# Kernel optimization log

Hardware: AMD Instinct MI355X
Metric: run time of the kernel (lower is better)

## Reference

```python
import jax, jax.numpy as jnp
import numpy as np

NU, NV = 8192, 8192
IN_DIM, HID, NCLS = 128, 64, 5


def setup_inputs() -> dict:
    key = jax.random.key(0)
    k1, k2, k3, k4, k5, k6, k7 = jax.random.split(key, 7)
    return {
        "u": jax.random.normal(k1, (NU, IN_DIM), dtype=jnp.float32),
        "v": jax.random.normal(k2, (NV, IN_DIM), dtype=jnp.float32),
        "adj": jax.random.uniform(k3, (NU, NV), dtype=jnp.float32),
        "degree": jax.random.uniform(k4, (NU + NV,), dtype=jnp.float32),
        "u_weight": jax.random.normal(k5, (NCLS, IN_DIM, HID), dtype=jnp.float32),
        "v_weight": jax.random.normal(k6, (NCLS, IN_DIM, HID), dtype=jnp.float32),
        "bias": jax.random.normal(k7, (HID,), dtype=jnp.float32),
        "r": 4,
    }


def reference(u, v, adj, degree, u_weight, v_weight, bias, r):
    # Sum weight slices for rating classes 0..r (r is a static Python int).
    Wu = jnp.sum(u_weight[: r + 1], axis=0)  # [IN_DIM, HID]
    Wv = jnp.sum(v_weight[: r + 1], axis=0)
    # Dropout is identity at p=0.0 (eval mode).
    su = u @ Wu  # [NU, HID]
    sv = v @ Wv  # [NV, HID]
    nu = adj.shape[0]
    # Block adjacency [[0, A], [A^T, 0]] row-scaled by diag(degree), applied to
    # concat(su, sv) -- computed block-wise, same math without the dense block matrix.
    top = degree[:nu, None] * (adj @ sv)      # [NU, HID]
    bot = degree[nu:, None] * (adj.T @ su)    # [NV, HID]
    return jnp.concatenate([top, bot], axis=0) + bias
```

## Files before the change

### kernel.cpp

```cpp
#include <hip/hip_runtime.h>
#include <stdint.h>


#define HID 64
#define IN_DIM 128
#define NROWS 8192
#define NCLS 5

typedef float f32x4 __attribute__((ext_vector_type(4)));
typedef short s16x8 __attribute__((ext_vector_type(8)));
typedef unsigned short u16;

static __device__ __forceinline__ short f2b(float x) {
    unsigned u = __builtin_bit_cast(unsigned, x);
    return (short)((u + 0x7FFFu + ((u >> 16) & 1u)) >> 16);
}

__global__ __launch_bounds__(256, 2) void k_prep(
    const float* __restrict__ u, const float* __restrict__ v,
    const float* __restrict__ uw, const float* __restrict__ vw,
    const int* __restrict__ rp, u16* __restrict__ ws)
{
    __shared__ float W[IN_DIM * HID];
    __shared__ float X[64 * 129];

    const int y = blockIdx.y;
    const float* __restrict__ src  = y ? v  : u;
    const float* __restrict__ wsrc = y ? vw : uw;
    u16* __restrict__ dstT = ws + (size_t)y * (HID * NROWS);
    const int i0 = blockIdx.x * 64;
    const int t = threadIdx.x;
    int r = *rp; if (r > NCLS - 1) r = NCLS - 1; if (r < 0) r = 0;

    for (int idx = t; idx < IN_DIM * HID; idx += 256) {
        float s = 0.f;
        for (int c = 0; c <= r; ++c) s += wsrc[c * (IN_DIM * HID) + idx];
        W[idx] = s;
    }
    #pragma unroll
    for (int qq = 0; qq < 8; ++qq) {
        int idx = t + qq * 256;
        int row = idx >> 5, c4 = idx & 31;
        f32x4 val = *(const f32x4*)&src[(size_t)(i0 + row) * IN_DIM + c4 * 4];
        float* d = &X[row * 129 + c4 * 4];
        d[0] = val[0]; d[1] = val[1]; d[2] = val[2]; d[3] = val[3];
    }
    __syncthreads();

    const int i = t & 63, h0 = (t >> 6) * 16;
    float acc[16];
    #pragma unroll
    for (int k = 0; k < 16; ++k) acc[k] = 0.f;
    for (int c = 0; c < IN_DIM; ++c) {
        float uv = X[i * 129 + c];
        const f32x4* wr = (const f32x4*)&W[c * HID + h0];
        f32x4 w0 = wr[0], w1 = wr[1], w2 = wr[2], w3 = wr[3];
        acc[0]  += uv * w0[0]; acc[1]  += uv * w0[1];
        acc[2]  += uv * w0[2]; acc[3]  += uv * w0[3];
        acc[4]  += uv * w1[0]; acc[5]  += uv * w1[1];
        acc[6]  += uv * w1[2]; acc[7]  += uv * w1[3];
        acc[8]  += uv * w2[0]; acc[9]  += uv * w2[1];
        acc[10] += uv * w2[2]; acc[11] += uv * w2[3];
        acc[12] += uv * w3[0]; acc[13] += uv * w3[1];
        acc[14] += uv * w3[2]; acc[15] += uv * w3[3];
    }
    #pragma unroll
    for (int hh = 0; hh < 16; ++hh)
        dstT[(size_t)(h0 + hh) * NROWS + i0 + i] = (u16)f2b(acc[hh]);
}

__global__ __launch_bounds__(256, 2) void k_main(
    const float* __restrict__ adj, const float* __restrict__ degree,
    const float* __restrict__ bias, const u16* __restrict__ ws,
    float* __restrict__ out)
{
    __shared__ float S[4][64 * 33];

    const int mode = blockIdx.y;
    const int bx = blockIdx.x;
    const int t = threadIdx.x;
    const int w = t >> 6, l = t & 63;
    const int q = l >> 4, l15 = l & 15;
    const int m0 = bx * 32;
    const unsigned a = (unsigned)(bx >> 1);
    const int kbase = w * 2048;
    const u16* __restrict__ BT = ws + (mode == 0 ? (size_t)(HID * NROWS) : 0);

    f32x4 acc[2][4];
    #pragma unroll
    for (int i = 0; i < 2; ++i)
        #pragma unroll
        for (int j = 0; j < 4; ++j) acc[i][j] = (f32x4){0.f, 0.f, 0.f, 0.f};

    if (mode == 0) {
        const float* __restrict__ ap0 = adj + (size_t)(m0 + l15) * NROWS;
        const float* __restrict__ ap1 = ap0 + (size_t)16 * NROWS;
        for (int tau = 0; tau < 32; ++tau) {
            const int k0 = kbase + (int)(((a + tau) & 31u) << 6);
            #pragma unroll
            for (int kh = 0; kh < 2; ++kh) {
                const int k = k0 + kh * 32 + q * 8;
                f32x4 a00 = *(const f32x4*)(ap0 + k);
                f32x4 a01 = *(const f32x4*)(ap0 + k + 4);
                f32x4 a10 = *(const f32x4*)(ap1 + k);
                f32x4 a11 = *(const f32x4*)(ap1 + k + 4);
                s16x8 bf[4];
                #pragma unroll
                for (int nn = 0; nn < 4; ++nn)
                    bf[nn] = *(const s16x8*)(BT + (size_t)(nn * 16 + l15) * NROWS + k);
                s16x8 af0, af1;
                af0[0]=f2b(a00[0]); af0[1]=f2b(a00[1]); af0[2]=f2b(a00[2]); af0[3]=f2b(a00[3]);
                af0[4]=f2b(a01[0]); af0[5]=f2b(a01[1]); af0[6]=f2b(a01[2]); af0[7]=f2b(a01[3]);
                af1[0]=f2b(a10[0]); af1[1]=f2b(a10[1]); af1[2]=f2b(a10[2]); af1[3]=f2b(a10[3]);
                af1[4]=f2b(a11[0]); af1[5]=f2b(a11[1]); af1[6]=f2b(a11[2]); af1[7]=f2b(a11[3]);
                #pragma unroll
                for (int nn = 0; nn < 4; ++nn) {
                    acc[0][nn] = __builtin_amdgcn_mfma_f32_16x16x32_bf16(af0, bf[nn], acc[0][nn], 0, 0, 0);
                    acc[1][nn] = __builtin_amdgcn_mfma_f32_16x16x32_bf16(af1, bf[nn], acc[1][nn], 0, 0, 0);
                }
            }
        }
    } else {
        float* __restrict__ T = S[w];
        const int wr_r = l >> 3;
        const int wr_c = (l & 7) * 4;
        const float* __restrict__ cb = adj + m0 + wr_c;
        for (int tau = 0; tau < 32; ++tau) {
            const int i0 = kbase + (int)(((a - tau) & 31u) << 6);
            f32x4 tr[8];
            #pragma unroll
            for (int c = 0; c < 8; ++c)
                tr[c] = *(const f32x4*)(cb + (size_t)(i0 + c * 8 + wr_r) * NROWS);
            #pragma unroll
            for (int c = 0; c < 8; ++c) {
                float* d = &T[(c * 8 + wr_r) * 33 + wr_c];
                d[0] = tr[c][0]; d[1] = tr[c][1]; d[2] = tr[c][2]; d[3] = tr[c][3];
            }
            asm volatile("s_waitcnt lgkmcnt(0)" ::: "memory");
            #pragma unroll
            for (int kh = 0; kh < 2; ++kh) {
                const int kk = i0 + kh * 32 + q * 8;
                s16x8 bf[4];
                #pragma unroll
                for (int nn = 0; nn < 4; ++nn)
                    bf[nn] = *(const s16x8*)(BT + (size_t)(nn * 16 + l15) * NROWS + kk);
                s16x8 af[2];
                #pragma unroll
                for (int mt = 0; mt < 2; ++mt) {
                    const int j = mt * 16 + l15;
                    #pragma unroll
                    for (int tt = 0; tt < 8; ++tt)
                        af[mt][tt] = f2b(T[(kh * 32 + q * 8 + tt) * 33 + j]);
                }
                #pragma unroll
                for (int nn = 0; nn < 4; ++nn) {
                    acc[0][nn] = __builtin_amdgcn_mfma_f32_16x16x32_bf16(af[0], bf[nn], acc[0][nn], 0, 0, 0);
                    acc[1][nn] = __builtin_amdgcn_mfma_f32_16x16x32_bf16(af[1], bf[nn], acc[1][nn], 0, 0, 0);
                }
            }
            asm volatile("" ::: "memory");
        }
    }

    asm volatile("" ::: "memory");
    {
        float* __restrict__ P = S[w];
        #pragma unroll
        for (int mt = 0; mt < 2; ++mt)
            #pragma unroll
            for (int nn = 0; nn < 4; ++nn)
                #pragma unroll
                for (int rg = 0; rg < 4; ++rg)
                    P[(mt * 16 + q * 4 + rg) * 64 + nn * 16 + l15] = acc[mt][nn][rg];
    }
    __syncthreads();

    const int e0 = t * 8;
    const int m = e0 >> 6, n = e0 & 63;
    f32x4 s0 = (f32x4){0.f,0.f,0.f,0.f}, s1 = s0;
    #pragma unroll
    for (int ww = 0; ww < 4; ++ww) {
        s0 += *(const f32x4*)&S[ww][e0];
        s1 += *(const f32x4*)&S[ww][e0 + 4];
    }
    const int grow = (mode ? NROWS : 0) + m0 + m;
    const float d = degree[grow];
    f32x4 b0 = *(const f32x4*)&bias[n];
    f32x4 b1 = *(const f32x4*)&bias[n + 4];
    f32x4 o0 = d * s0 + b0;
    f32x4 o1 = d * s1 + b1;
    *(f32x4*)&out[(size_t)grow * HID + n]     = o0;
    *(f32x4*)&out[(size_t)grow * HID + n + 4] = o1;
}

extern "C" void kernel_launch(void* const* d_in, const int* in_sizes, int n_in,
                              void* d_out, int out_size, void* d_ws, size_t ws_size,
                              hipStream_t stream) {
    (void)in_sizes; (void)n_in; (void)out_size; (void)ws_size;
    const float* u      = (const float*)d_in[0];
    const float* v      = (const float*)d_in[1];
    const float* adj    = (const float*)d_in[2];
    const float* degree = (const float*)d_in[3];
    const float* uw     = (const float*)d_in[4];
    const float* vw     = (const float*)d_in[5];
    const float* bias   = (const float*)d_in[6];
    const int*   rp     = (const int*)d_in[7];
    u16*   ws  = (u16*)d_ws;
    float* out = (float*)d_out;

    k_prep<<<dim3(128, 2), 256, 0, stream>>>(u, v, uw, vw, rp, ws);
    k_main<<<dim3(256, 2), 256, 0, stream>>>(adj, degree, bias, ws, out);
}
```

Before: 481.6 us.

## Read adj once, emit bf16 transposed tiles for the bottom product

The fused two-mode kernel is split into k_top and k_bot. k_top streams fp32 adj rows once for adj@sv, converts them to bf16, transposes them through swizzled LDS, and writes a blocked bf16 copy of adj^T to workspace. k_bot then computes adj^T@su from that half-size bf16 copy instead of rereading fp32 adj with column-strided loads. The top path also prefetches the next tile into registers and shrinks row tiles to 16. The cost is an extra 128MB bf16 write plus read, one more launch, and a dependency between the two kernels.

```diff
diff --git a/kernel.cpp b/kernel.cpp
--- a/kernel.cpp
+++ b/kernel.cpp
@@ -69,128 +69,175 @@
         dstT[(size_t)(h0 + hh) * NROWS + i0 + i] = (u16)f2b(acc[hh]);
 }
 
-__global__ __launch_bounds__(256, 2) void k_main(
+__global__ __launch_bounds__(256, 2) void k_top(
     const float* __restrict__ adj, const float* __restrict__ degree,
     const float* __restrict__ bias, const u16* __restrict__ ws,
-    float* __restrict__ out)
+    u16* __restrict__ wt, float* __restrict__ out)
 {
-    __shared__ float S[4][64 * 33];
-
-    const int mode = blockIdx.y;
+    __shared__ u16  Tt[4][16 * 64];
+    __shared__ float S[4][16 * 64];
+
     const int bx = blockIdx.x;
     const int t = threadIdx.x;
     const int w = t >> 6, l = t & 63;
     const int q = l >> 4, l15 = l & 15;
-    const int m0 = bx * 32;
-    const unsigned a = (unsigned)(bx >> 1);
+    const int m0 = bx * 16;
     const int kbase = w * 2048;
-    const u16* __restrict__ BT = ws + (mode == 0 ? (size_t)(HID * NROWS) : 0);
-
-    f32x4 acc[2][4];
-    #pragma unroll
-    for (int i = 0; i < 2; ++i)
-        #pragma unroll
-        for (int j = 0; j < 4; ++j) acc[i][j] = (f32x4){0.f, 0.f, 0.f, 0.f};
-
-    if (mode == 0) {
-        const float* __restrict__ ap0 = adj + (size_t)(m0 + l15) * NROWS;
-        const float* __restrict__ ap1 = ap0 + (size_t)16 * NROWS;
-        for (int tau = 0; tau < 32; ++tau) {
-            const int k0 = kbase + (int)(((a + tau) & 31u) << 6);
-            #pragma unroll
-            for (int kh = 0; kh < 2; ++kh) {
-                const int k = k0 + kh * 32 + q * 8;
-                f32x4 a00 = *(const f32x4*)(ap0 + k);
-                f32x4 a01 = *(const f32x4*)(ap0 + k + 4);
-                f32x4 a10 = *(const f32x4*)(ap1 + k);
-                f32x4 a11 = *(const f32x4*)(ap1 + k + 4);
-                s16x8 bf[4];
-                #pragma unroll
-                for (int nn = 0; nn < 4; ++nn)
-                    bf[nn] = *(const s16x8*)(BT + (size_t)(nn * 16 + l15) * NROWS + k);
-                s16x8 af0, af1;
-                af0[0]=f2b(a00[0]); af0[1]=f2b(a00[1]); af0[2]=f2b(a00[2]); af0[3]=f2b(a00[3]);
-                af0[4]=f2b(a01[0]); af0[5]=f2b(a01[1]); af0[6]=f2b(a01[2]); af0[7]=f2b(a01[3]);
-                af1[0]=f2b(a10[0]); af1[1]=f2b(a10[1]); af1[2]=f2b(a10[2]); af1[3]=f2b(a10[3]);
-                af1[4]=f2b(a11[0]); af1[5]=f2b(a11[1]); af1[6]=f2b(a11[2]); af1[7]=f2b(a11[3]);
-                #pragma unroll
-                for (int nn = 0; nn < 4; ++nn) {
-                    acc[0][nn] = __builtin_amdgcn_mfma_f32_16x16x32_bf16(af0, bf[nn], acc[0][nn], 0, 0, 0);
-                    acc[1][nn] = __builtin_amdgcn_mfma_f32_16x16x32_bf16(af1, bf[nn], acc[1][nn], 0, 0, 0);
-                }
-            }
-        }
-    } else {
-        float* __restrict__ T = S[w];
-        const int wr_r = l >> 3;
-        const int wr_c = (l & 7) * 4;
-        const float* __restrict__ cb = adj + m0 + wr_c;
-        for (int tau = 0; tau < 32; ++tau) {
-            const int i0 = kbase + (int)(((a - tau) & 31u) << 6);
-            f32x4 tr[8];
-            #pragma unroll
-            for (int c = 0; c < 8; ++c)
-                tr[c] = *(const f32x4*)(cb + (size_t)(i0 + c * 8 + wr_r) * NROWS);
-            #pragma unroll
-            for (int c = 0; c < 8; ++c) {
-                float* d = &T[(c * 8 + wr_r) * 33 + wr_c];
-                d[0] = tr[c][0]; d[1] = tr[c][1]; d[2] = tr[c][2]; d[3] = tr[c][3];
-            }
-            asm volatile("s_waitcnt lgkmcnt(0)" ::: "memory");
-            #pragma unroll
-            for (int kh = 0; kh < 2; ++kh) {
-                const int kk = i0 + kh * 32 + q * 8;
-                s16x8 bf[4];
-                #pragma unroll
-                for (int nn = 0; nn < 4; ++nn)
-                    bf[nn] = *(const s16x8*)(BT + (size_t)(nn * 16 + l15) * NROWS + kk);
-                s16x8 af[2];
-                #pragma unroll
-                for (int mt = 0; mt < 2; ++mt) {
-                    const int j = mt * 16 + l15;
-                    #pragma unroll
-                    for (int tt = 0; tt < 8; ++tt)
-                        af[mt][tt] = f2b(T[(kh * 32 + q * 8 + tt) * 33 + j]);
-                }
-                #pragma unroll
-                for (int nn = 0; nn < 4; ++nn) {
-                    acc[0][nn] = __builtin_amdgcn_mfma_f32_16x16x32_bf16(af[0], bf[nn], acc[0][nn], 0, 0, 0);
-                    acc[1][nn] = __builtin_amdgcn_mfma_f32_16x16x32_bf16(af[1], bf[nn], acc[1][nn], 0, 0, 0);
-                }
-            }
-            asm volatile("" ::: "memory");
-        }
+    const u16* __restrict__ BT = ws + (size_t)HID * NROWS;
+    const float* __restrict__ ap0 = adj + (size_t)(m0 + l15) * NROWS + q * 8;
+    u16* __restrict__ Tw = Tt[w];
+
+    f32x4 acc[4];
+    #pragma unroll
+    for (int nn = 0; nn < 4; ++nn) acc[nn] = (f32x4){0.f, 0.f, 0.f, 0.f};
+
+    f32x4 c00 = *(const f32x4*)(ap0 + kbase);
+    f32x4 c01 = *(const f32x4*)(ap0 + kbase + 4);
+    f32x4 c10 = *(const f32x4*)(ap0 + kbase + 32);
+    f32x4 c11 = *(const f32x4*)(ap0 + kbase + 36);
+
+    for (int tau = 0; tau < 32; ++tau) {
+        const int k0c = kbase + tau * 64;
+        const int knx = kbase + ((tau + 1) & 31) * 64;
+        f32x4 n00 = *(const f32x4*)(ap0 + knx);
+        f32x4 n01 = *(const f32x4*)(ap0 + knx + 4);
+        f32x4 n10 = *(const f32x4*)(ap0 + knx + 32);
+        f32x4 n11 = *(const f32x4*)(ap0 + knx + 36);
+
+        s16x8 af0;
+        af0[0]=f2b(c00[0]); af0[1]=f2b(c00[1]); af0[2]=f2b(c00[2]); af0[3]=f2b(c00[3]);
+        af0[4]=f2b(c01[0]); af0[5]=f2b(c01[1]); af0[6]=f2b(c01[2]); af0[7]=f2b(c01[3]);
+        *(s16x8*)&Tw[l15 * 64 + ((q ^ (l15 & 7)) * 8)] = af0;
+        {
+            s16x8 bf[4];
+            #pragma unroll
+            for (int nn = 0; nn < 4; ++nn)
+                bf[nn] = *(const s16x8*)(BT + (size_t)(nn * 16 + l15) * NROWS + k0c + q * 8);
+            #pragma unroll
+            for (int nn = 0; nn < 4; ++nn)
+                acc[nn] = __builtin_amdgcn_mfma_f32_16x16x32_bf16(af0, bf[nn], acc[nn], 0, 0, 0);
+        }
+        s16x8 af1;
+        af1[0]=f2b(c10[0]); af1[1]=f2b(c10[1]); af1[2]=f2b(c10[2]); af1[3]=f2b(c10[3]);
+        af1[4]=f2b(c11[0]); af1[5]=f2b(c11[1]); af1[6]=f2b(c11[2]); af1[7]=f2b(c11[3]);
+        *(s16x8*)&Tw[l15 * 64 + (((4 + q) ^ (l15 & 7)) * 8)] = af1;
+        {
+            s16x8 bf[4];
+            #pragma unroll
+            for (int nn = 0; nn < 4; ++nn)
+                bf[nn] = *(const s16x8*)(BT + (size_t)(nn * 16 + l15) * NROWS + k0c + 32 + q * 8);
+            #pragma unroll
+            for (int nn = 0; nn < 4; ++nn)
+                acc[nn] = __builtin_amdgcn_mfma_f32_16x16x32_bf16(af1, bf[nn], acc[nn], 0, 0, 0);
+        }
+
+        asm volatile("s_waitcnt lgkmcnt(0)" ::: "memory");
+
+        s16x8 p0, p1;
+        #pragma unroll
+        for (int ii = 0; ii < 8; ++ii)
+            p0[ii] = (short)Tw[ii * 64 + (((l >> 3) ^ ii) & 7) * 8 + (l & 7)];
+        #pragma unroll
+        for (int ii = 0; ii < 8; ++ii)
+            p1[ii] = (short)Tw[(ii + 8) * 64 + (((l >> 3) ^ ii) & 7) * 8 + (l & 7)];
+
+        u16* dst = wt + (size_t)((k0c >> 4) + (l >> 4)) * (NROWS * 16)
+                      + (size_t)bx * 256 + (size_t)(l & 15) * 16;
+        *(s16x8*)dst       = p0;
+        *(s16x8*)(dst + 8) = p1;
+
+        asm volatile("" ::: "memory");
+        c00 = n00; c01 = n01; c10 = n10; c11 = n11;
     }
 
     asm volatile("" ::: "memory");
     {
         float* __restrict__ P = S[w];
         #pragma unroll
-        for (int mt = 0; mt < 2; ++mt)
-            #pragma unroll
-            for (int nn = 0; nn < 4; ++nn)
-                #pragma unroll
-                for (int rg = 0; rg < 4; ++rg)
-                    P[(mt * 16 + q * 4 + rg) * 64 + nn * 16 + l15] = acc[mt][nn][rg];
+        for (int nn = 0; nn < 4; ++nn)
+            #pragma unroll
+            for (int rg = 0; rg < 4; ++rg)
+                P[(q * 4 + rg) * 64 + nn * 16 + l15] = acc[nn][rg];
     }
     __syncthreads();
 
-    const int e0 = t * 8;
+    const int e0 = t * 4;
     const int m = e0 >> 6, n = e0 & 63;
-    f32x4 s0 = (f32x4){0.f,0.f,0.f,0.f}, s1 = s0;
-    #pragma unroll
-    for (int ww = 0; ww < 4; ++ww) {
-        s0 += *(const f32x4*)&S[ww][e0];
-        s1 += *(const f32x4*)&S[ww][e0 + 4];
-    }
-    const int grow = (mode ? NROWS : 0) + m0 + m;
+    f32x4 s = (f32x4){0.f, 0.f, 0.f, 0.f};
+    #pragma unroll
+    for (int ww = 0; ww < 4; ++ww) s += *(const f32x4*)&S[ww][e0];
+    const int grow = m0 + m;
     const float d = degree[grow];
-    f32x4 b0 = *(const f32x4*)&bias[n];
-    f32x4 b1 = *(const f32x4*)&bias[n + 4];
-    f32x4 o0 = d * s0 + b0;
-    f32x4 o1 = d * s1 + b1;
-    *(f32x4*)&out[(size_t)grow * HID + n]     = o0;
-    *(f32x4*)&out[(size_t)grow * HID + n + 4] = o1;
+    f32x4 b = *(const f32x4*)&bias[n];
+    *(f32x4*)&out[(size_t)grow * HID + n] = d * s + b;
+}
+
+__global__ __launch_bounds__(256, 2) void k_bot(
+    const float* __restrict__ degree, const float* __restrict__ bias,
+    const u16* __restrict__ ws, const u16* __restrict__ wt,
+    float* __restrict__ out)
+{
+    __shared__ float S[4][16 * 64];
+
+    const int bx = blockIdx.x;
+    const int t = threadIdx.x;
+    const int w = t >> 6, l = t & 63;
+    const int q = l >> 4, l15 = l & 15;
+    const int m0 = bx * 16;
+    const int kbase = w * 2048;
+    const u16* __restrict__ BT = ws;
+    const u16* __restrict__ PB = wt + (size_t)bx * (NROWS * 16)
+                                    + (size_t)l15 * 16 + (size_t)(q & 1) * 8;
+
+    f32x4 acc[4];
+    #pragma unroll
+    for (int nn = 0; nn < 4; ++nn) acc[nn] = (f32x4){0.f, 0.f, 0.f, 0.f};
+
+    for (int tau = 0; tau < 32; ++tau) {
+        const int i0 = kbase + tau * 64;
+        const int ib0 = (i0 >> 4) + (q >> 1);
+        {
+            s16x8 af = *(const s16x8*)(PB + (size_t)ib0 * 256);
+            s16x8 bf[4];
+            #pragma unroll
+            for (int nn = 0; nn < 4; ++nn)
+                bf[nn] = *(const s16x8*)(BT + (size_t)(nn * 16 + l15) * NROWS + i0 + q * 8);
+            #pragma unroll
+            for (int nn = 0; nn < 4; ++nn)
+                acc[nn] = __builtin_amdgcn_mfma_f32_16x16x32_bf16(af, bf[nn], acc[nn], 0, 0, 0);
+        }
+        {
+            s16x8 af = *(const s16x8*)(PB + (size_t)(ib0 + 2) * 256);
+            s16x8 bf[4];
+            #pragma unroll
+            for (int nn = 0; nn < 4; ++nn)
+                bf[nn] = *(const s16x8*)(BT + (size_t)(nn * 16 + l15) * NROWS + i0 + 32 + q * 8);
+            #pragma unroll
+            for (int nn = 0; nn < 4; ++nn)
+                acc[nn] = __builtin_amdgcn_mfma_f32_16x16x32_bf16(af, bf[nn], acc[nn], 0, 0, 0);
+        }
+    }
+
+    asm volatile("" ::: "memory");
+    {
+        float* __restrict__ P = S[w];
+        #pragma unroll
+        for (int nn = 0; nn < 4; ++nn)
+            #pragma unroll
+            for (int rg = 0; rg < 4; ++rg)
+                P[(q * 4 + rg) * 64 + nn * 16 + l15] = acc[nn][rg];
+    }
+    __syncthreads();
+
+    const int e0 = t * 4;
+    const int m = e0 >> 6, n = e0 & 63;
+    f32x4 s = (f32x4){0.f, 0.f, 0.f, 0.f};
+    #pragma unroll
+    for (int ww = 0; ww < 4; ++ww) s += *(const f32x4*)&S[ww][e0];
+    const int grow = NROWS + m0 + m;
+    const float d = degree[grow];
+    f32x4 b = *(const f32x4*)&bias[n];
+    *(f32x4*)&out[(size_t)grow * HID + n] = d * s + b;
 }
 
 extern "C" void kernel_launch(void* const* d_in, const int* in_sizes, int n_in,
@@ -206,8 +253,10 @@
     const float* bias   = (const float*)d_in[6];
     const int*   rp     = (const int*)d_in[7];
     u16*   ws  = (u16*)d_ws;
+    u16*   wt  = ws + 1048576;
     float* out = (float*)d_out;
 
     k_prep<<<dim3(128, 2), 256, 0, stream>>>(u, v, uw, vw, rp, ws);
-    k_main<<<dim3(256, 2), 256, 0, stream>>>(adj, degree, bias, ws, out);
-}
+    k_top <<<dim3(512),    256, 0, stream>>>(adj, degree, bias, ws, wt, out);
+    k_bot <<<dim3(512),    256, 0, stream>>>(degree, bias, ws, wt, out);
+}
```

After: 595.9 us. +23.7%, slower.
